# Performance work log

Hardware: AMD Instinct MI355X
Metric: run time of the kernel (lower is better)

## Reference

```python
import jax, jax.numpy as jnp
import numpy as np
from jax import lax

GAMMA = 1.0  # init kwarg

def setup_inputs() -> dict:
    key = jax.random.key(0)
    k1, k2 = jax.random.split(key)
    B, L, D = 64, 256, 1024
    return {
        "student_tokens": jax.random.normal(k1, (B, L, D), jnp.float32),
        "teacher_tokens": jax.random.normal(k2, (B, L, D), jnp.float32),
    }

def _soft_dtw(dist, gamma):
    # dist: (B, LS, LT). Returns R[:, LS, LT] of the soft-DTW DP.
    B, LS, LT = dist.shape
    inf = jnp.array(jnp.inf, dist.dtype)

    def cell(r_left, inputs):
        d, r_diag, r_up = inputs  # each (B,)
        stacked = jnp.stack([r_diag, r_up, r_left], axis=-1)  # (B, 3)
        softmin = -gamma * jax.nn.logsumexp(-stacked / gamma, axis=-1)
        r = d + softmin
        return r, r

    def row_step(prev_row, dist_row):
        # prev_row: (B, LT+1) = R[i-1, :]; dist_row: (B, LT) = dist[:, i-1, :]
        xs = (dist_row.T, prev_row[:, :-1].T, prev_row[:, 1:].T)  # each (LT, B)
        r0 = jnp.full((B,), inf, dist.dtype)  # R[i, 0] = inf
        _, row = lax.scan(cell, r0, xs)  # (LT, B)
        new_row = jnp.concatenate([r0[:, None], row.T], axis=1)  # (B, LT+1)
        return new_row, None

    init_row = jnp.concatenate(
        [jnp.zeros((B, 1), dist.dtype), jnp.full((B, LT), inf, dist.dtype)], axis=1
    )  # R[0, :] = [0, inf, ..., inf]
    final_row, _ = lax.scan(row_step, init_row, jnp.swapaxes(dist, 0, 1))
    return final_row[:, -1]  # R[:, LS, LT]

def reference(student_tokens, teacher_tokens):
    # torch.cdist(p=2) via the expanded quadratic form (avoids (B,L,L,D) blowup)
    s2 = jnp.sum(student_tokens * student_tokens, axis=-1)  # (B, LS)
    t2 = jnp.sum(teacher_tokens * teacher_tokens, axis=-1)  # (B, LT)
    sq = (s2[:, :, None] + t2[:, None, :]
          - 2.0 * jnp.einsum('bld,bmd->blm', student_tokens, teacher_tokens))
    dist = jnp.sqrt(jnp.maximum(sq, 1e-12))  # (B, LS, LT)
    return _soft_dtw(dist, GAMMA).mean()
```

## Files before the change

### kernel.cpp

```cpp
#include <hip/hip_runtime.h>
#include <math.h>

#define BB 64
#define LL 256
#define DD 1024
#define NDPAD 512
#define BK 32
#define LOG2E 1.4426950408889634f
#define LN2   0.6931471805599453f

typedef __attribute__((ext_vector_type(8))) short short8v;
typedef __attribute__((ext_vector_type(4))) float float4v;

__device__ __forceinline__ unsigned short f2bf(float f) {
    unsigned u = __float_as_uint(f);
    unsigned r = (u + 0x7fffu + ((u >> 16) & 1u)) >> 16;
    return (unsigned short)r;
}
__device__ __forceinline__ float bf2f(unsigned short u) {
    return __uint_as_float(((unsigned)u) << 16);
}

__global__ __launch_bounds__(256) void fused_kernel(const float* __restrict__ S,
                                                    const float* __restrict__ T,
                                                    unsigned short* __restrict__ Dd) {
    __shared__ unsigned short lds[2][2][128 * BK];
    __shared__ float nrm[2][128];

    const int b    = blockIdx.x;
    const int tile = blockIdx.y;
    const int i0 = (tile & 1) * 128;
    const int j0 = (tile >> 1) * 128;
    const int tid = threadIdx.x, w = tid >> 6, lane = tid & 63;
    const int wr = w >> 1, wc = w & 1;

    const float* Sg = S + ((size_t)b * LL + i0) * DD;
    const float* Tg = T + ((size_t)b * LL + j0) * DD;

    const int sr   = w * 16 + (lane >> 2);
    const int slot = lane & 3;
    const int kb   = slot ^ (sr & 3);

    float4v acc[4][4];
    const float4v fzero = {0.f, 0.f, 0.f, 0.f};
    #pragma unroll
    for (int mi = 0; mi < 4; ++mi)
        #pragma unroll
        for (int ni = 0; ni < 4; ++ni) acc[mi][ni] = fzero;

    struct StgSet { float4 a[2][2]; float4 bb[2][2]; };
    StgSet st0, st1;
    float ns[2][2] = {};

    auto issue = [&](StgSet& st, int kt) {
        const float* pa = Sg + (size_t)sr * DD + kt * BK + kb * 8;
        const float* pb = Tg + (size_t)sr * DD + kt * BK + kb * 8;
        st.a[0][0]  = *(const float4*)(pa);
        st.a[0][1]  = *(const float4*)(pa + 4);
        st.a[1][0]  = *(const float4*)(pa + 64 * DD);
        st.a[1][1]  = *(const float4*)(pa + 64 * DD + 4);
        st.bb[0][0] = *(const float4*)(pb);
        st.bb[0][1] = *(const float4*)(pb + 4);
        st.bb[1][0] = *(const float4*)(pb + 64 * DD);
        st.bb[1][1] = *(const float4*)(pb + 64 * DD + 4);
    };

    auto cvtwrite = [&](const float4& v0, const float4& v1, unsigned short* dst, float& nacc) {
        nacc += v0.x * v0.x + v0.y * v0.y + v0.z * v0.z + v0.w * v0.w
              + v1.x * v1.x + v1.y * v1.y + v1.z * v1.z + v1.w * v1.w;
        uint4 o;
        o.x = ((unsigned)f2bf(v0.y) << 16) | f2bf(v0.x);
        o.y = ((unsigned)f2bf(v0.w) << 16) | f2bf(v0.z);
        o.z = ((unsigned)f2bf(v1.y) << 16) | f2bf(v1.x);
        o.w = ((unsigned)f2bf(v1.w) << 16) | f2bf(v1.z);
        *(uint4*)dst = o;
    };

    auto commit = [&](StgSet& st, int buf) {
        #pragma unroll
        for (int n = 0; n < 2; ++n) {
            cvtwrite(st.a[n][0],  st.a[n][1],  &lds[buf][0][(n * 64 + sr) * BK + slot * 8], ns[0][n]);
            cvtwrite(st.bb[n][0], st.bb[n][1], &lds[buf][1][(n * 64 + sr) * BK + slot * 8], ns[1][n]);
        }
    };

    auto compute = [&](int buf) {
        const unsigned short* LA = &lds[buf][0][0];
        const unsigned short* LB = &lds[buf][1][0];
        short8v af[4], bf[4];
        #pragma unroll
        for (int mi = 0; mi < 4; ++mi) {
            int row = wr * 64 + mi * 16 + (lane & 15);
            int kbf = (lane >> 4) ^ (row & 3);
            af[mi] = *(const short8v*)(LA + row * BK + kbf * 8);
        }
        #pragma unroll
        for (int ni = 0; ni < 4; ++ni) {
            int row = wc * 64 + ni * 16 + (lane & 15);
            int kbf = (lane >> 4) ^ (row & 3);
            bf[ni] = *(const short8v*)(LB + row * BK + kbf * 8);
        }
        #pragma unroll
        for (int mi = 0; mi < 4; ++mi)
            #pragma unroll
            for (int ni = 0; ni < 4; ++ni)
                acc[mi][ni] = __builtin_amdgcn_mfma_f32_16x16x32_bf16(af[mi], bf[ni],
                                                                      acc[mi][ni], 0, 0, 0);
    };

    issue(st0, 0);
    for (int kt2 = 0; kt2 < 32; kt2 += 2) {
        issue(st1, kt2 + 1);
        commit(st0, 0);
        __syncthreads();
        compute(0);
        if (kt2 + 2 < 32) issue(st0, kt2 + 2);
        commit(st1, 1);
        __syncthreads();
        compute(1);
    }

    #pragma unroll
    for (int side = 0; side < 2; ++side)
        #pragma unroll
        for (int n = 0; n < 2; ++n) {
            float s = ns[side][n];
            s += __shfl_xor(s, 1, 64);
            s += __shfl_xor(s, 2, 64);
            if (slot == 0) nrm[side][n * 64 + sr] = s;
        }
    __syncthreads();

    const int r0 = (lane >> 4) * 4;
    const int cf = lane & 15;
    unsigned short* Db = Dd + (size_t)b * NDPAD * 256;
    #pragma unroll
    for (int mi = 0; mi < 4; ++mi) {
        #pragma unroll
        for (int ni = 0; ni < 4; ++ni) {
            int lj = wc * 64 + ni * 16 + cf;
            float tj = nrm[1][lj];
            int j = j0 + lj;
            #pragma unroll
            for (int rg = 0; rg < 4; ++rg) {
                int li = wr * 64 + mi * 16 + r0 + rg;
                float sq = nrm[0][li] + tj - 2.0f * acc[mi][ni][rg];
                float dv = sqrtf(fmaxf(sq, 1e-12f));
                int i = i0 + li;
                Db[(size_t)(i + j) * 256 + j] = f2bf(dv * LOG2E);
            }
        }
    }
}


__device__ __forceinline__ float wshr1(float src, float fill) {
    return __int_as_float(__builtin_amdgcn_update_dpp(
        __float_as_int(fill), __float_as_int(src), 0x138, 0xF, 0xF, false));
}

__global__ __launch_bounds__(256) void sdtw_kernel(const unsigned short* __restrict__ Dg,
                                                   float* __restrict__ res) {
    __shared__ unsigned short sd[8][16 * 256];
    __shared__ float bbuf[3][2][16];
    const int b = blockIdx.x;
    const int tid = threadIdx.x;
    const int w = tid >> 6;
    const int lane = tid & 63;
    const float INF = INFINITY;
    const unsigned short* Db = Dg + (size_t)b * NDPAD * 256;

    auto prefetch = [&](int c) {
        #pragma unroll
        for (int q = 0; q < 8; ++q) {
            __builtin_amdgcn_global_load_lds(
                (const __attribute__((address_space(1))) void*)(Db + (size_t)c * 4096 + q * 512 + lane * 8),
                (__attribute__((address_space(3))) void*)(&sd[c & 7][q * 512]),
                16, 0, 0);
        }
    };

    const int col0 = 64 * w + lane;
    float rm1 = INF, rm2 = INF;
    float p2carry = (tid == 0) ? 0.0f : INF;
    float bcarry = INF;

    if (w == 0) {
        prefetch(0);
        prefetch(1);
        asm volatile("s_waitcnt vmcnt(8)" ::: "memory");
    }
    asm volatile("s_waitcnt lgkmcnt(0)" ::: "memory");
    __builtin_amdgcn_s_barrier();

    for (int r = 0; r < 35; ++r) {
        if (w == 0 && r + 2 < 32) prefetch(r + 2);
        const int c = r - w;
        if (0 <= c && c < 32) {
            const unsigned short* Lp = &sd[c & 7][0];
            float dv[16];
            #pragma unroll
            for (int q = 0; q < 16; ++q)
                dv[q] = bf2f(Lp[q * 256 + col0]);

            float bv[16];
            if (w == 0) {
                #pragma unroll
                for (int q = 0; q < 16; ++q) bv[q] = INF;
            } else {
                const float4* bp4 = (const float4*)&bbuf[w - 1][c & 1][0];
                float4 b0 = bp4[0], b1 = bp4[1], b2 = bp4[2], b3 = bp4[3];
                bv[0] = bcarry;
                bv[1] = b0.x;  bv[2] = b0.y;  bv[3] = b0.z;  bv[4] = b0.w;
                bv[5] = b1.x;  bv[6] = b1.y;  bv[7] = b1.z;  bv[8] = b1.w;
                bv[9] = b2.x;  bv[10] = b2.y; bv[11] = b2.z; bv[12] = b2.w;
                bv[13] = b3.x; bv[14] = b3.y; bv[15] = b3.z;
                bcarry = b3.w;
            }
            asm volatile("s_waitcnt lgkmcnt(0)" ::: "memory");
            __builtin_amdgcn_sched_barrier(0);

            const int ibase = 16 * c - col0;
            float bb[16];
            #pragma unroll
            for (int q = 0; q < 16; ++q) {
                float p1 = wshr1(rm1, bv[q]);
                float p2 = p2carry;
                p2carry = p1;
                float m   = fminf(p2, fminf(rm1, p1));
                float mid = __builtin_amdgcn_fmed3f(p2, rm1, p1);
                float M   = fmaxf(p2, fmaxf(rm1, p1));
                float s   = (__builtin_amdgcn_exp2f(m - mid) +
                             __builtin_amdgcn_exp2f(m - M)) + 1.0f;
                float rcv = dv[q] + m - __builtin_amdgcn_logf(s);
                bool valid = (unsigned)(ibase + q) < 256u;
                rcv = valid ? rcv : INF;
                rm2 = rm1;
                rm1 = rcv;
                bb[q] = rcv;
            }
            if (w < 3 && lane == 63) {
                float4* op = (float4*)&bbuf[w][c & 1][0];
                op[0] = make_float4(bb[0], bb[1], bb[2], bb[3]);
                op[1] = make_float4(bb[4], bb[5], bb[6], bb[7]);
                op[2] = make_float4(bb[8], bb[9], bb[10], bb[11]);
                op[3] = make_float4(bb[12], bb[13], bb[14], bb[15]);
            }
        }
        if (w == 0) {
            if (r < 30) asm volatile("s_waitcnt vmcnt(8)" ::: "memory");
            else        asm volatile("s_waitcnt vmcnt(0)" ::: "memory");
        }
        asm volatile("s_waitcnt lgkmcnt(0)" ::: "memory");
        __builtin_amdgcn_s_barrier();
    }
    if (tid == 255) res[b] = rm2 * LN2;
}

__global__ void reduce_kernel(const float* __restrict__ res, float* __restrict__ out) {
    int t = threadIdx.x;
    float v = res[t];
    #pragma unroll
    for (int off = 32; off; off >>= 1) v += __shfl_down(v, off, 64);
    if (t == 0) out[0] = v * (1.0f / BB);
}

extern "C" void kernel_launch(void* const* d_in, const int* in_sizes, int n_in,
                              void* d_out, int out_size, void* d_ws, size_t ws_size,
                              hipStream_t stream) {
    const float* S = (const float*)d_in[0];
    const float* T = (const float*)d_in[1];

    const size_t nDiag = (size_t)BB * NDPAD * 256;
    unsigned short* diag = (unsigned short*)d_ws;
    float* rsv = (float*)(diag + nDiag);

    fused_kernel<<<dim3(BB, 4), 256, 0, stream>>>(S, T, diag);
    sdtw_kernel<<<BB, 256, 0, stream>>>(diag, rsv);
    reduce_kernel<<<1, 64, 0, stream>>>(rsv, (float*)d_out);
}
```

Before: 82.72 us.

## Widen distance GEMM tile to 128x256 with 512 threads and padded LDS

The fused distance kernel now computes a 128x256 output tile per block using 8 waves, so each block covers all teacher rows and the grid shrinks from 256 to 128 blocks. Each student row tile is loaded once instead of twice, which cuts redundant global reads of S and the repeated bf16 conversion and norm work. The LDS row stride is padded from 32 to 36 elements to reduce bank conflicts, and the B-side staging swizzle is reworked for two threads per row. The trade-off is fewer blocks (128) spread over many compute units, which leaves some units idle, plus more LDS per block.

```diff
diff --git a/kernel.cpp b/kernel.cpp
--- a/kernel.cpp
+++ b/kernel.cpp
@@ -6,6 +6,7 @@
 #define DD 1024
 #define NDPAD 512
 #define BK 32
+#define BKS 36
 #define LOG2E 1.4426950408889634f
 #define LN2   0.6931471805599453f
 
@@ -21,25 +22,28 @@
     return __uint_as_float(((unsigned)u) << 16);
 }
 
-__global__ __launch_bounds__(256) void fused_kernel(const float* __restrict__ S,
+__global__ __launch_bounds__(512) void fused_kernel(const float* __restrict__ S,
                                                     const float* __restrict__ T,
                                                     unsigned short* __restrict__ Dd) {
-    __shared__ unsigned short lds[2][2][128 * BK];
-    __shared__ float nrm[2][128];
+    __shared__ unsigned short ldsA[2][128 * BKS];
+    __shared__ unsigned short ldsB[2][256 * BKS];
+    __shared__ float nrmA[128];
+    __shared__ float nrmB[256];
 
     const int b    = blockIdx.x;
-    const int tile = blockIdx.y;
-    const int i0 = (tile & 1) * 128;
-    const int j0 = (tile >> 1) * 128;
+    const int half = blockIdx.y;
+    const int i0   = half * 128;
     const int tid = threadIdx.x, w = tid >> 6, lane = tid & 63;
-    const int wr = w >> 1, wc = w & 1;
+    const int wr = w >> 2, wc = w & 3;
 
     const float* Sg = S + ((size_t)b * LL + i0) * DD;
-    const float* Tg = T + ((size_t)b * LL + j0) * DD;
-
-    const int sr   = w * 16 + (lane >> 2);
-    const int slot = lane & 3;
-    const int kb   = slot ^ (sr & 3);
+    const float* Tg = T + (size_t)b * LL * DD;
+
+    const int rowA = tid >> 2, slotA = tid & 3;
+    const int kbA  = slotA ^ (rowA & 3);
+    const int rowB = tid >> 1, sB = tid & 1;
+    const int mB   = (2 * sB) ^ (rowB & 2);
+    const int dB0  = mB ^ (rowB & 3);
 
     float4v acc[4][4];
     const float4v fzero = {0.f, 0.f, 0.f, 0.f};
@@ -48,21 +52,19 @@
         #pragma unroll
         for (int ni = 0; ni < 4; ++ni) acc[mi][ni] = fzero;
 
-    struct StgSet { float4 a[2][2]; float4 bb[2][2]; };
-    StgSet st0, st1;
-    float ns[2][2] = {};
-
-    auto issue = [&](StgSet& st, int kt) {
-        const float* pa = Sg + (size_t)sr * DD + kt * BK + kb * 8;
-        const float* pb = Tg + (size_t)sr * DD + kt * BK + kb * 8;
-        st.a[0][0]  = *(const float4*)(pa);
-        st.a[0][1]  = *(const float4*)(pa + 4);
-        st.a[1][0]  = *(const float4*)(pa + 64 * DD);
-        st.a[1][1]  = *(const float4*)(pa + 64 * DD + 4);
-        st.bb[0][0] = *(const float4*)(pb);
-        st.bb[0][1] = *(const float4*)(pb + 4);
-        st.bb[1][0] = *(const float4*)(pb + 64 * DD);
-        st.bb[1][1] = *(const float4*)(pb + 64 * DD + 4);
+    struct Stg { float4 a0, a1, b0, b1, b2, b3; };
+    Stg st0, st1;
+    float nsA = 0.0f, nsB = 0.0f;
+
+    auto issue = [&](Stg& st, int kt) {
+        const float* pa = Sg + (size_t)rowA * DD + kt * BK + kbA * 8;
+        st.a0 = *(const float4*)(pa);
+        st.a1 = *(const float4*)(pa + 4);
+        const float* pb = Tg + (size_t)rowB * DD + kt * BK + mB * 8;
+        st.b0 = *(const float4*)(pb);
+        st.b1 = *(const float4*)(pb + 4);
+        st.b2 = *(const float4*)(pb + 8);
+        st.b3 = *(const float4*)(pb + 12);
     };
 
     auto cvtwrite = [&](const float4& v0, const float4& v1, unsigned short* dst, float& nacc) {
@@ -76,29 +78,25 @@
         *(uint4*)dst = o;
     };
 
-    auto commit = [&](StgSet& st, int buf) {
-        #pragma unroll
-        for (int n = 0; n < 2; ++n) {
-            cvtwrite(st.a[n][0],  st.a[n][1],  &lds[buf][0][(n * 64 + sr) * BK + slot * 8], ns[0][n]);
-            cvtwrite(st.bb[n][0], st.bb[n][1], &lds[buf][1][(n * 64 + sr) * BK + slot * 8], ns[1][n]);
-        }
+    auto commit = [&](Stg& st, int buf) {
+        cvtwrite(st.a0, st.a1, &ldsA[buf][rowA * BKS + slotA * 8], nsA);
+        cvtwrite(st.b0, st.b1, &ldsB[buf][rowB * BKS + dB0 * 8], nsB);
+        cvtwrite(st.b2, st.b3, &ldsB[buf][rowB * BKS + (dB0 ^ 1) * 8], nsB);
     };
 
     auto compute = [&](int buf) {
-        const unsigned short* LA = &lds[buf][0][0];
-        const unsigned short* LB = &lds[buf][1][0];
         short8v af[4], bf[4];
         #pragma unroll
         for (int mi = 0; mi < 4; ++mi) {
             int row = wr * 64 + mi * 16 + (lane & 15);
             int kbf = (lane >> 4) ^ (row & 3);
-            af[mi] = *(const short8v*)(LA + row * BK + kbf * 8);
+            af[mi] = *(const short8v*)(&ldsA[buf][row * BKS + kbf * 8]);
         }
         #pragma unroll
         for (int ni = 0; ni < 4; ++ni) {
             int row = wc * 64 + ni * 16 + (lane & 15);
             int kbf = (lane >> 4) ^ (row & 3);
-            bf[ni] = *(const short8v*)(LB + row * BK + kbf * 8);
+            bf[ni] = *(const short8v*)(&ldsB[buf][row * BKS + kbf * 8]);
         }
         #pragma unroll
         for (int mi = 0; mi < 4; ++mi)
@@ -120,15 +118,15 @@
         compute(1);
     }
 
-    #pragma unroll
-    for (int side = 0; side < 2; ++side)
-        #pragma unroll
-        for (int n = 0; n < 2; ++n) {
-            float s = ns[side][n];
-            s += __shfl_xor(s, 1, 64);
-            s += __shfl_xor(s, 2, 64);
-            if (slot == 0) nrm[side][n * 64 + sr] = s;
-        }
+    {
+        float s = nsA;
+        s += __shfl_xor(s, 1, 64);
+        s += __shfl_xor(s, 2, 64);
+        if (slotA == 0) nrmA[rowA] = s;
+        float t = nsB;
+        t += __shfl_xor(t, 1, 64);
+        if (sB == 0) nrmB[rowB] = t;
+    }
     __syncthreads();
 
     const int r0 = (lane >> 4) * 4;
@@ -139,12 +137,12 @@
         #pragma unroll
         for (int ni = 0; ni < 4; ++ni) {
             int lj = wc * 64 + ni * 16 + cf;
-            float tj = nrm[1][lj];
-            int j = j0 + lj;
+            float tj = nrmB[lj];
+            int j = lj;
             #pragma unroll
             for (int rg = 0; rg < 4; ++rg) {
                 int li = wr * 64 + mi * 16 + r0 + rg;
-                float sq = nrm[0][li] + tj - 2.0f * acc[mi][ni][rg];
+                float sq = nrmA[li] + tj - 2.0f * acc[mi][ni][rg];
                 float dv = sqrtf(fmaxf(sq, 1e-12f));
                 int i = i0 + li;
                 Db[(size_t)(i + j) * 256 + j] = f2bf(dv * LOG2E);
@@ -275,7 +273,7 @@
     unsigned short* diag = (unsigned short*)d_ws;
     float* rsv = (float*)(diag + nDiag);
 
-    fused_kernel<<<dim3(BB, 4), 256, 0, stream>>>(S, T, diag);
+    fused_kernel<<<dim3(BB, 2), 512, 0, stream>>>(S, T, diag);
     sdtw_kernel<<<BB, 256, 0, stream>>>(diag, rsv);
     reduce_kernel<<<1, 64, 0, stream>>>(rsv, (float*)d_out);
 }
```

New measurement: 97.01 us. +17.3%, slower.

## Shrink GEMM tiles to 64x64 for more blocks and use packed bf16 convert

Applied to the files above, without the earlier changes.

The distance GEMM kernel now uses 64x64 output tiles instead of 128x128, launching 1024 blocks instead of 256 so the 256 CUs are better filled. The LDS swizzle is adjusted to the new row mapping, and f32-to-bf16 conversion now uses the hardware v_cvt_pk_bf16_f32 instruction instead of manual rounding. Smaller tiles mean each S/T row is loaded from global memory four times instead of twice, raising global traffic and lowering MFMA reuse per load.

```diff
diff --git a/kernel.cpp b/kernel.cpp
--- a/kernel.cpp
+++ b/kernel.cpp
@@ -20,90 +20,88 @@
 __device__ __forceinline__ float bf2f(unsigned short u) {
     return __uint_as_float(((unsigned)u) << 16);
 }
+__device__ __forceinline__ unsigned cvtpk(float lo, float hi) {
+    unsigned r;
+    asm("v_cvt_pk_bf16_f32 %0, %1, %2" : "=v"(r) : "v"(lo), "v"(hi));
+    return r;
+}
 
 __global__ __launch_bounds__(256) void fused_kernel(const float* __restrict__ S,
                                                     const float* __restrict__ T,
                                                     unsigned short* __restrict__ Dd) {
-    __shared__ unsigned short lds[2][2][128 * BK];
-    __shared__ float nrm[2][128];
+    __shared__ unsigned short lds[2][2][64 * BK];
+    __shared__ float nrm[2][64];
 
     const int b    = blockIdx.x;
     const int tile = blockIdx.y;
-    const int i0 = (tile & 1) * 128;
-    const int j0 = (tile >> 1) * 128;
+    const int i0 = (tile & 3) * 64;
+    const int j0 = (tile >> 2) * 64;
     const int tid = threadIdx.x, w = tid >> 6, lane = tid & 63;
     const int wr = w >> 1, wc = w & 1;
 
     const float* Sg = S + ((size_t)b * LL + i0) * DD;
     const float* Tg = T + ((size_t)b * LL + j0) * DD;
 
-    const int sr   = w * 16 + (lane >> 2);
-    const int slot = lane & 3;
-    const int kb   = slot ^ (sr & 3);
-
-    float4v acc[4][4];
+    const int sr   = tid >> 2;
+    const int slot = tid & 3;
+    const int kb   = slot ^ ((sr >> 1) & 3);
+
+    float4v acc[2][2];
     const float4v fzero = {0.f, 0.f, 0.f, 0.f};
     #pragma unroll
-    for (int mi = 0; mi < 4; ++mi)
-        #pragma unroll
-        for (int ni = 0; ni < 4; ++ni) acc[mi][ni] = fzero;
-
-    struct StgSet { float4 a[2][2]; float4 bb[2][2]; };
-    StgSet st0, st1;
-    float ns[2][2] = {};
-
-    auto issue = [&](StgSet& st, int kt) {
+    for (int mi = 0; mi < 2; ++mi)
+        #pragma unroll
+        for (int ni = 0; ni < 2; ++ni) acc[mi][ni] = fzero;
+
+    struct Stg { float4 a0, a1, b0, b1; };
+    Stg st0, st1;
+    float nsA = 0.0f, nsB = 0.0f;
+
+    auto issue = [&](Stg& s, int kt) {
         const float* pa = Sg + (size_t)sr * DD + kt * BK + kb * 8;
         const float* pb = Tg + (size_t)sr * DD + kt * BK + kb * 8;
-        st.a[0][0]  = *(const float4*)(pa);
-        st.a[0][1]  = *(const float4*)(pa + 4);
-        st.a[1][0]  = *(const float4*)(pa + 64 * DD);
-        st.a[1][1]  = *(const float4*)(pa + 64 * DD + 4);
-        st.bb[0][0] = *(const float4*)(pb);
-        st.bb[0][1] = *(const float4*)(pb + 4);
-        st.bb[1][0] = *(const float4*)(pb + 64 * DD);
-        st.bb[1][1] = *(const float4*)(pb + 64 * DD + 4);
+        s.a0 = *(const float4*)(pa);
+        s.a1 = *(const float4*)(pa + 4);
+        s.b0 = *(const float4*)(pb);
+        s.b1 = *(const float4*)(pb + 4);
     };
 
     auto cvtwrite = [&](const float4& v0, const float4& v1, unsigned short* dst, float& nacc) {
         nacc += v0.x * v0.x + v0.y * v0.y + v0.z * v0.z + v0.w * v0.w
               + v1.x * v1.x + v1.y * v1.y + v1.z * v1.z + v1.w * v1.w;
         uint4 o;
-        o.x = ((unsigned)f2bf(v0.y) << 16) | f2bf(v0.x);
-        o.y = ((unsigned)f2bf(v0.w) << 16) | f2bf(v0.z);
-        o.z = ((unsigned)f2bf(v1.y) << 16) | f2bf(v1.x);
-        o.w = ((unsigned)f2bf(v1.w) << 16) | f2bf(v1.z);
+        o.x = cvtpk(v0.x, v0.y);
+        o.y = cvtpk(v0.z, v0.w);
+        o.z = cvtpk(v1.x, v1.y);
+        o.w = cvtpk(v1.z, v1.w);
         *(uint4*)dst = o;
     };
 
-    auto commit = [&](StgSet& st, int buf) {
-        #pragma unroll
-        for (int n = 0; n < 2; ++n) {
-            cvtwrite(st.a[n][0],  st.a[n][1],  &lds[buf][0][(n * 64 + sr) * BK + slot * 8], ns[0][n]);
-            cvtwrite(st.bb[n][0], st.bb[n][1], &lds[buf][1][(n * 64 + sr) * BK + slot * 8], ns[1][n]);
-        }
+    auto commit = [&](Stg& s, int buf) {
+        cvtwrite(s.a0, s.a1, &lds[buf][0][sr * BK + slot * 8], nsA);
+        cvtwrite(s.b0, s.b1, &lds[buf][1][sr * BK + slot * 8], nsB);
     };
 
     auto compute = [&](int buf) {
         const unsigned short* LA = &lds[buf][0][0];
         const unsigned short* LB = &lds[buf][1][0];
-        short8v af[4], bf[4];
-        #pragma unroll
-        for (int mi = 0; mi < 4; ++mi) {
-            int row = wr * 64 + mi * 16 + (lane & 15);
-            int kbf = (lane >> 4) ^ (row & 3);
+        short8v af[2], bf[2];
+        #pragma unroll
+        for (int mi = 0; mi < 2; ++mi) {
+            int row = wr * 32 + mi * 16 + (lane & 15);
+            int kbf = (lane >> 4) ^ ((row >> 1) & 3);
             af[mi] = *(const short8v*)(LA + row * BK + kbf * 8);
         }
         #pragma unroll
-        for (int ni = 0; ni < 4; ++ni) {
-            int row = wc * 64 + ni * 16 + (lane & 15);
-            int kbf = (lane >> 4) ^ (row & 3);
+        for (int ni = 0; ni < 2; ++ni) {
+            int row = wc * 32 + ni * 16 + (lane & 15);
+            int kbf = (lane >> 4) ^ ((row >> 1) & 3);
             bf[ni] = *(const short8v*)(LB + row * BK + kbf * 8);
         }
         #pragma unroll
-        for (int mi = 0; mi < 4; ++mi)
-            #pragma unroll
-            for (int ni = 0; ni < 4; ++ni)
+        for (int mi = 0; mi < 2; ++mi)
+            #pragma unroll
+            for (int ni = 0; ni < 2; ++ni)
                 acc[mi][ni] = __builtin_amdgcn_mfma_f32_16x16x32_bf16(af[mi], bf[ni],
                                                                       acc[mi][ni], 0, 0, 0);
     };
@@ -120,30 +118,31 @@
         compute(1);
     }
 
-    #pragma unroll
-    for (int side = 0; side < 2; ++side)
-        #pragma unroll
-        for (int n = 0; n < 2; ++n) {
-            float s = ns[side][n];
-            s += __shfl_xor(s, 1, 64);
-            s += __shfl_xor(s, 2, 64);
-            if (slot == 0) nrm[side][n * 64 + sr] = s;
-        }
+    {
+        float s = nsA;
+        s += __shfl_xor(s, 1, 64);
+        s += __shfl_xor(s, 2, 64);
+        if (slot == 0) nrm[0][sr] = s;
+        float t = nsB;
+        t += __shfl_xor(t, 1, 64);
+        t += __shfl_xor(t, 2, 64);
+        if (slot == 0) nrm[1][sr] = t;
+    }
     __syncthreads();
 
     const int r0 = (lane >> 4) * 4;
     const int cf = lane & 15;
     unsigned short* Db = Dd + (size_t)b * NDPAD * 256;
     #pragma unroll
-    for (int mi = 0; mi < 4; ++mi) {
-        #pragma unroll
-        for (int ni = 0; ni < 4; ++ni) {
-            int lj = wc * 64 + ni * 16 + cf;
+    for (int mi = 0; mi < 2; ++mi) {
+        #pragma unroll
+        for (int ni = 0; ni < 2; ++ni) {
+            int lj = wc * 32 + ni * 16 + cf;
             float tj = nrm[1][lj];
             int j = j0 + lj;
             #pragma unroll
             for (int rg = 0; rg < 4; ++rg) {
-                int li = wr * 64 + mi * 16 + r0 + rg;
+                int li = wr * 32 + mi * 16 + r0 + rg;
                 float sq = nrm[0][li] + tj - 2.0f * acc[mi][ni][rg];
                 float dv = sqrtf(fmaxf(sq, 1e-12f));
                 int i = i0 + li;
@@ -152,7 +151,6 @@
         }
     }
 }
-
 
 __device__ __forceinline__ float wshr1(float src, float fill) {
     return __int_as_float(__builtin_amdgcn_update_dpp(
@@ -275,7 +273,7 @@
     unsigned short* diag = (unsigned short*)d_ws;
     float* rsv = (float*)(diag + nDiag);
 
-    fused_kernel<<<dim3(BB, 4), 256, 0, stream>>>(S, T, diag);
+    fused_kernel<<<dim3(BB, 16), 256, 0, stream>>>(S, T, diag);
     sdtw_kernel<<<BB, 256, 0, stream>>>(diag, rsv);
     reduce_kernel<<<1, 64, 0, stream>>>(rsv, (float*)d_out);
 }
```

Measured after the change: 81.20 us. About the same (-1.8%).
